# Kernel tuning notes

Measured on AMD Instinct MI355X. Metric: run time of the kernel, lower is better.

The kernel has to match this reference:

```python
import jax, jax.numpy as jnp
import numpy as np

DIM = 1024
N_HEADS = 16
HEAD_DIM = DIM // N_HEADS
MAX_SEQ = 2048
B, S = 4, 2048


def _rope_tables(seq_len):
    inv_freq = 1.0 / (10000.0 ** (jnp.arange(0, HEAD_DIM, 2, dtype=jnp.float32) / HEAD_DIM))
    t = jnp.arange(seq_len, dtype=jnp.float32)
    freqs = jnp.outer(t, inv_freq)            # [S, HEAD_DIM/2]
    emb = jnp.concatenate([freqs, freqs], -1)  # [S, HEAD_DIM]
    return jnp.cos(emb), jnp.sin(emb)


def _apply_rope(x, cos, sin):
    # x: [B, S, H, Dh]; cos/sin: [S, Dh]
    c = cos[None, :, None, :]
    s = sin[None, :, None, :]
    x1, x2 = jnp.split(x, 2, axis=-1)
    x_rot = jnp.concatenate([-x2, x1], -1)
    return x * c + x_rot * s


def setup_inputs() -> dict:
    key = jax.random.key(0)
    kx, kq, kk, kv, ko = jax.random.split(key, 5)
    std = DIM ** -0.5
    x = jax.random.normal(kx, (B, S, DIM), jnp.float32)
    Wq = jax.random.normal(kq, (DIM, DIM), jnp.float32) * std
    Wk = jax.random.normal(kk, (DIM, DIM), jnp.float32) * std
    Wv = jax.random.normal(kv, (DIM, DIM), jnp.float32) * std
    Wo = jax.random.normal(ko, (DIM, DIM), jnp.float32) * std
    # causal mask: 1 where attending is allowed, 0 where masked (mask==0 -> -inf)
    mask = jnp.tril(jnp.ones((S, S), jnp.int32))[None, None]  # [1,1,S,S]
    return {"x": x, "Wq": Wq, "Wk": Wk, "Wv": Wv, "Wo": Wo, "mask": mask}


def reference(x, Wq, Wk, Wv, Wo, mask) -> jnp.ndarray:
    b, s, _ = x.shape
    scale = HEAD_DIM ** -0.5
    # torch Linear: y = x @ W.T, W is [out, in]
    q = (x @ Wq.T).reshape(b, s, N_HEADS, HEAD_DIM)
    k = (x @ Wk.T).reshape(b, s, N_HEADS, HEAD_DIM)
    v = (x @ Wv.T).reshape(b, s, N_HEADS, HEAD_DIM)
    cos, sin = _rope_tables(s)
    q = _apply_rope(q, cos, sin)
    k = _apply_rope(k, cos, sin)
    # [B, H, S, S]
    attn = jnp.einsum('bqhd,bkhd->bhqk', q, k) * scale
    attn = jnp.where(mask == 0, -jnp.inf, attn)
    attn = jax.nn.softmax(attn, axis=-1)
    out = jnp.einsum('bhqk,bkhd->bqhd', attn, v).reshape(b, s, DIM)
    return out @ Wo.T
```

## Files before the change

### kernel.cpp

```cpp
#include <hip/hip_runtime.h>
#include <hip/hip_bf16.h>
#include <math.h>

using bf16 = __hip_bfloat16;
typedef __attribute__((ext_vector_type(8))) short short8;
typedef __attribute__((ext_vector_type(4))) float float4v;

#define DIM 1024
#define NH 16
#define HD 64
#define BB 4
#define SS 2048
#define MTOT (BB * SS)

#define ROPE_LOG2 0.41524101186092034f
#define PC1 0.18033688f
#define PC0 -23.08312066f

__device__ inline short bf16bits(float x) {
  return __builtin_bit_cast(short, __float2bfloat16(x));
}
__device__ inline float bits2f(unsigned short b) {
  return __builtin_bit_cast(float, (unsigned)b << 16);
}
__device__ inline unsigned pack2(float a, float b) {
  return (unsigned)(unsigned short)bf16bits(a) |
         ((unsigned)(unsigned short)bf16bits(b) << 16);
}

__device__ inline void async16(const void* g, void* l) {
  __builtin_amdgcn_global_load_lds(
      (const __attribute__((address_space(1))) void*)g,
      (__attribute__((address_space(3))) void*)l, 16, 0, 0);
}

__device__ inline void cvt8(const float* __restrict__ in, bf16* __restrict__ out,
                            size_t i) {
  const float4v* p = (const float4v*)in + i * 2;
  float4v a = p[0], b = p[1];
  short8 r;
  r[0] = bf16bits(a[0]); r[1] = bf16bits(a[1]);
  r[2] = bf16bits(a[2]); r[3] = bf16bits(a[3]);
  r[4] = bf16bits(b[0]); r[5] = bf16bits(b[1]);
  r[6] = bf16bits(b[2]); r[7] = bf16bits(b[3]);
  ((short8*)out)[i] = r;
}

__global__ __launch_bounds__(256) void prep(
    const float* __restrict__ x, const float* __restrict__ w0,
    const float* __restrict__ w1, const float* __restrict__ w2,
    const float* __restrict__ w3, bf16* __restrict__ xb, bf16* __restrict__ o0,
    bf16* __restrict__ o1, bf16* __restrict__ o2, bf16* __restrict__ o3,
    unsigned* __restrict__ tab) {
  const int bid = blockIdx.x;
  const int tid = threadIdx.x;
  if (bid < 4096) {
    cvt8(x, xb, (size_t)bid * 256 + tid);
  } else if (bid < 6144) {
    int wsel = (bid - 4096) >> 9;
    const float* in = wsel == 0 ? w0 : wsel == 1 ? w1 : wsel == 2 ? w2 : w3;
    bf16* out = wsel == 0 ? o0 : wsel == 1 ? o1 : wsel == 2 ? o2 : o3;
    cvt8(in, out, (size_t)((bid - 4096) & 511) * 256 + tid);
  } else {
    int i = (bid - 6144) * 256 + tid;
    int s = i >> 5, d = i & 31;
    float inv = exp2f(-(float)d * ROPE_LOG2);
    float sn, cs;
    sincosf((float)s * inv, &sn, &cs);
    tab[i] = pack2(cs, sn);
  }
}

__global__ __launch_bounds__(256, 3) void gemm_qkv(
    const bf16* __restrict__ A, const bf16* __restrict__ W,
    bf16* __restrict__ Cbase, const unsigned* __restrict__ rt) {
  __shared__ __align__(16) short sPool[4][4096];
  short* sT = &sPool[0][0];

  const int tid = threadIdx.x;
  const int wave = tid >> 6;
  const int lane = tid & 63;
  const int l15 = lane & 15;
  const int quad = lane >> 4;
  const int m0 = blockIdx.x * 128;
  const int n0 = blockIdx.y * 128;
  const int wm = (wave >> 1) * 64;
  const int wn = (wave & 1) * 64;
  const int K = DIM;

  float4v acc[4][4];
#pragma unroll
  for (int i = 0; i < 4; i++)
#pragma unroll
    for (int j = 0; j < 4; j++)
#pragma unroll
      for (int r = 0; r < 4; r++) acc[i][j][r] = 0.0f;

  auto stage = [&](int buf, int k0) {
    short* dA = &sPool[buf * 2][0];
    short* dB = &sPool[buf * 2 + 1][0];
#pragma unroll
    for (int i = 0; i < 2; i++) {
      int c0 = i * 256 + wave * 64;
      int c = c0 + lane;
      int row = c >> 2, cb = c & 3;
      async16(A + (size_t)(m0 + row) * K + k0 + cb * 8, dA + c0 * 8);
      async16(W + (size_t)(n0 + row) * K + k0 + cb * 8, dB + c0 * 8);
    }
  };

  stage(0, 0);
  __syncthreads();

  int cur = 0;
  for (int k0 = 0; k0 < K; k0 += 32, cur ^= 1) {
    if (k0 + 32 < K) stage(cur ^ 1, k0 + 32);

    const short* sA = &sPool[cur * 2][0];
    const short* sB = &sPool[cur * 2 + 1][0];
    short8 af[4], bfr[4];
#pragma unroll
    for (int mi = 0; mi < 4; mi++)
      af[mi] = *(const short8*)(sA + (wm + mi * 16 + l15) * 32 + quad * 8);
#pragma unroll
    for (int ni = 0; ni < 4; ni++)
      bfr[ni] = *(const short8*)(sB + (wn + ni * 16 + l15) * 32 + quad * 8);
#pragma unroll
    for (int mi = 0; mi < 4; mi++)
#pragma unroll
      for (int ni = 0; ni < 4; ni++)
        acc[mi][ni] = __builtin_amdgcn_mfma_f32_16x16x32_bf16(
            af[mi], bfr[ni], acc[mi][ni], 0, 0, 0);

    __syncthreads();
  }

  const int third = n0 >> 10;
  const int nloc = n0 & 1023;
  bf16* C = Cbase + (size_t)third * MTOT * DIM;

  if (third == 2) {
    const int bb_ = m0 >> 11;
    const int s0 = m0 & (SS - 1);
    const int h0 = nloc >> 6;
#pragma unroll
    for (int half = 0; half < 2; half++) {
      if (half) __syncthreads();
      if ((wave & 1) == half) {
#pragma unroll
        for (int mi = 0; mi < 4; mi++)
#pragma unroll
          for (int ni = 0; ni < 4; ni++)
#pragma unroll
            for (int r = 0; r < 4; r++)
              sT[(ni * 16 + l15) * 130 + wm + mi * 16 + quad * 4 + r] =
                  bf16bits(acc[mi][ni][r]);
      }
      __syncthreads();
      int row = tid >> 2, cb = tid & 3;
      size_t base =
          ((size_t)(bb_ * NH + h0 + half) * HD + row) * SS + s0 + cb * 32;
#pragma unroll
      for (int c = 0; c < 4; c++) {
        short8 vv = *(const short8*)(sT + row * 130 + cb * 32 + c * 8);
        *(short8*)((short*)C + base + c * 8) = vv;
      }
    }
    return;
  }

#pragma unroll
  for (int mi = 0; mi < 4; mi++) {
#pragma unroll
    for (int r = 0; r < 4; r++) {
      int m = m0 + wm + mi * 16 + quad * 4 + r;
      int b = m >> 11;
      int s = m & (SS - 1);
      int h = (nloc + wn) >> 6;
      bf16* outp = C + ((size_t)(b * NH + h) * SS + s) * HD;
#pragma unroll
      for (int ni = 0; ni < 2; ni++) {
        int d = ni * 16 + l15;
        unsigned cspack = rt[s * 32 + d];
        float cs = bits2f((unsigned short)(cspack & 0xffff));
        float sn = bits2f((unsigned short)(cspack >> 16));
        float lo = acc[mi][ni][r];
        float hi = acc[mi][ni + 2][r];
        outp[d] = __float2bfloat16(lo * cs - hi * sn);
        outp[d + 32] = __float2bfloat16(hi * cs + lo * sn);
      }
    }
  }
}

__global__ __launch_bounds__(256, 3) void gemm_out(const bf16* __restrict__ A,
                                                   const bf16* __restrict__ W,
                                                   float* __restrict__ C) {
  __shared__ __align__(16) short sPool[4][4096];

  const int tid = threadIdx.x;
  const int wave = tid >> 6;
  const int lane = tid & 63;
  const int l15 = lane & 15;
  const int quad = lane >> 4;
  const int m0 = blockIdx.x * 128;
  const int n0 = blockIdx.y * 128;
  const int wm = (wave >> 1) * 64;
  const int wn = (wave & 1) * 64;
  const int K = DIM, N = DIM;

  float4v acc[4][4];
#pragma unroll
  for (int i = 0; i < 4; i++)
#pragma unroll
    for (int j = 0; j < 4; j++)
#pragma unroll
      for (int r = 0; r < 4; r++) acc[i][j][r] = 0.0f;

  auto stage = [&](int buf, int k0) {
    short* dA = &sPool[buf * 2][0];
    short* dB = &sPool[buf * 2 + 1][0];
#pragma unroll
    for (int i = 0; i < 2; i++) {
      int c0 = i * 256 + wave * 64;
      int c = c0 + lane;
      int row = c >> 2, cb = c & 3;
      async16(A + (size_t)(m0 + row) * K + k0 + cb * 8, dA + c0 * 8);
      async16(W + (size_t)(n0 + row) * K + k0 + cb * 8, dB + c0 * 8);
    }
  };

  stage(0, 0);
  __syncthreads();

  int cur = 0;
  for (int k0 = 0; k0 < K; k0 += 32, cur ^= 1) {
    if (k0 + 32 < K) stage(cur ^ 1, k0 + 32);

    const short* sA = &sPool[cur * 2][0];
    const short* sB = &sPool[cur * 2 + 1][0];
    short8 af[4], bfr[4];
#pragma unroll
    for (int mi = 0; mi < 4; mi++)
      af[mi] = *(const short8*)(sA + (wm + mi * 16 + l15) * 32 + quad * 8);
#pragma unroll
    for (int ni = 0; ni < 4; ni++)
      bfr[ni] = *(const short8*)(sB + (wn + ni * 16 + l15) * 32 + quad * 8);
#pragma unroll
    for (int mi = 0; mi < 4; mi++)
#pragma unroll
      for (int ni = 0; ni < 4; ni++)
        acc[mi][ni] = __builtin_amdgcn_mfma_f32_16x16x32_bf16(
            af[mi], bfr[ni], acc[mi][ni], 0, 0, 0);

    __syncthreads();
  }

#pragma unroll
  for (int mi = 0; mi < 4; mi++) {
#pragma unroll
    for (int r = 0; r < 4; r++) {
      int m = m0 + wm + mi * 16 + quad * 4 + r;
#pragma unroll
      for (int ni = 0; ni < 4; ni++) {
        int n = n0 + wn + ni * 16 + l15;
        C[(size_t)m * N + n] = acc[mi][ni][r];
      }
    }
  }
}

#define SKV 64
#define SP 64

__global__ __launch_bounds__(512, 2) void attn_fwd(const bf16* __restrict__ q,
                                                   const bf16* __restrict__ k,
                                                   const bf16* __restrict__ vt,
                                                   bf16* __restrict__ o) {
  __shared__ __align__(16) short sK[2][64 * SKV];
  __shared__ __align__(16) short sV[2][64 * SKV];
  __shared__ __align__(16) short sP[8][16 * SP];

  const int tid = threadIdx.x;
  const int wave = tid >> 6;
  const int g = wave >> 2;
  const int wv = wave & 3;
  const int lane = tid & 63;
  const int l15 = lane & 15;
  const int quad = lane >> 4;
  const int bh = blockIdx.x;
  const int p = blockIdx.y;
  const int qt[4] = {g == 0 ? p : 7 - p, g == 0 ? 15 - p : 8 + p,
                     g == 0 ? 16 + p : 23 - p, g == 0 ? 31 - p : 24 + p};
  const int maxkt = 31 - p;
  const size_t hb = (size_t)bh * SS * HD;
  const size_t vtb = (size_t)bh * HD * SS;

  short8 aQ[4][2];
#pragma unroll
  for (int ti = 0; ti < 4; ti++) {
    const bf16* qp =
        q + hb + (size_t)(qt[ti] * 64 + wv * 16 + l15) * HD + quad * 8;
    aQ[ti][0] = *(const short8*)qp;
    aQ[ti][1] = *(const short8*)(qp + 32);
  }

  float l_part[4] = {0.0f, 0.0f, 0.0f, 0.0f};
  float4v acc_o[4][4];
#pragma unroll
  for (int ti = 0; ti < 4; ti++)
#pragma unroll
    for (int di = 0; di < 4; di++)
#pragma unroll
      for (int r = 0; r < 4; r++) acc_o[ti][di][r] = 0.0f;

  int4 kr, vr;
  auto load_kv = [&](int kt_) {
    int k0n = kt_ * 64;
    int c = tid;
    kr = *(const int4*)(k + hb + (size_t)(k0n + (c >> 3)) * HD + (c & 7) * 8);
    vr = *(const int4*)(vt + vtb + (size_t)(c >> 3) * SS + k0n + (c & 7) * 8);
  };
  auto stage_write = [&](int buf) {
    int c = tid;
    int row = c >> 3;
    int sl = (c & 7) ^ (row & 7);
    *(int4*)(&sK[buf][row * SKV + sl * 8]) = kr;
    *(int4*)(&sV[buf][row * SKV + sl * 8]) = vr;
  };

  load_kv(0);
  stage_write(0);
  __syncthreads();

  for (int kt = 0; kt <= maxkt; kt++) {
    const int cur = kt & 1;
    if (kt < maxkt) load_kv(kt + 1);

    short8 kf[8], vf[8];
#pragma unroll
    for (int t = 0; t < 2; t++)
#pragma unroll
      for (int i = 0; i < 4; i++) {
        int row = i * 16 + l15;
        int sl = (t * 4 + quad) ^ (l15 & 7);
        kf[t * 4 + i] = *(const short8*)(&sK[cur][row * SKV + sl * 8]);
        vf[t * 4 + i] = *(const short8*)(&sV[cur][row * SKV + sl * 8]);
      }

    const int k0 = kt * 64;
    short* pw = &sP[wave][0];
#pragma unroll
    for (int ti = 0; ti < 4; ti++) {
      if (kt <= qt[ti]) {
        float4v s[4];
#pragma unroll
        for (int ni = 0; ni < 4; ni++)
#pragma unroll
          for (int r = 0; r < 4; r++) s[ni][r] = 0.0f;
        __builtin_amdgcn_s_setprio(1);
#pragma unroll
        for (int t = 0; t < 2; t++)
#pragma unroll
          for (int ni = 0; ni < 4; ni++)
            s[ni] = __builtin_amdgcn_mfma_f32_16x16x32_bf16(
                kf[t * 4 + ni], aQ[ti][t], s[ni], 0, 0, 0);
        __builtin_amdgcn_s_setprio(0);

        const bool diag = (kt == qt[ti]);
        const int qglob = qt[ti] * 64 + wv * 16 + l15;
#pragma unroll
        for (int ni = 0; ni < 4; ni++) {
          float pe[4];
#pragma unroll
          for (int r = 0; r < 4; r++) {
            float x = exp2f(fmaf(s[ni][r], PC1, PC0));
            if (diag && (k0 + ni * 16 + quad * 4 + r > qglob)) x = 0.0f;
            l_part[ti] += x;
            pe[r] = x;
          }
          int2 w2;
          w2.x = (int)pack2(pe[0], pe[1]);
          w2.y = (int)pack2(pe[2], pe[3]);
          int slw = (2 * ni + (quad >> 1)) ^ (l15 & 7);
          *(int2*)(pw + l15 * SP + slw * 8 + (quad & 1) * 4) = w2;
        }
        asm volatile("s_waitcnt lgkmcnt(0)" ::: "memory");

        __builtin_amdgcn_s_setprio(1);
#pragma unroll
        for (int t = 0; t < 2; t++) {
          int slr = (t * 4 + quad) ^ (l15 & 7);
          short8 aP = *(const short8*)(pw + l15 * SP + slr * 8);
#pragma unroll
          for (int di = 0; di < 4; di++)
            acc_o[ti][di] = __builtin_amdgcn_mfma_f32_16x16x32_bf16(
                aP, vf[t * 4 + di], acc_o[ti][di], 0, 0, 0);
        }
        __builtin_amdgcn_s_setprio(0);
      }
    }

    if (kt < maxkt) stage_write(cur ^ 1);
    __syncthreads();
  }

  const int b = bh >> 4, h = bh & 15;
#pragma unroll
  for (int ti = 0; ti < 4; ti++) {
    float lr = l_part[ti];
    lr += __shfl_xor(lr, 16, 64);
    lr += __shfl_xor(lr, 32, 64);
#pragma unroll
    for (int r = 0; r < 4; r++) {
      float invl = 1.0f / __shfl(lr, quad * 4 + r, 64);
      bf16* op =
          o + (size_t)(b * SS + qt[ti] * 64 + wv * 16 + quad * 4 + r) * DIM +
          h * HD;
#pragma unroll
      for (int di = 0; di < 4; di++)
        op[di * 16 + l15] = __float2bfloat16(acc_o[ti][di][r] * invl);
    }
  }
}

extern "C" void kernel_launch(void* const* d_in, const int* in_sizes, int n_in,
                              void* d_out, int out_size, void* d_ws,
                              size_t ws_size, hipStream_t stream) {
  const float* x = (const float*)d_in[0];
  const float* Wq = (const float*)d_in[1];
  const float* Wk = (const float*)d_in[2];
  const float* Wv = (const float*)d_in[3];
  const float* Wo = (const float*)d_in[4];
  float* out = (float*)d_out;

  char* ws = (char*)d_ws;
  const size_t xsz = (size_t)MTOT * DIM * sizeof(bf16);
  bf16* xb = (bf16*)ws;
  bf16* qb_ = (bf16*)(ws + xsz);
  bf16* kb = (bf16*)(ws + 2 * xsz);
  bf16* vtb = (bf16*)(ws + 3 * xsz);
  bf16* wqb = (bf16*)(ws + 4 * xsz);
  bf16* wkb = wqb + (size_t)DIM * DIM;
  bf16* wvb = wkb + (size_t)DIM * DIM;
  bf16* wob = wvb + (size_t)DIM * DIM;
  unsigned* rt = (unsigned*)(wob + (size_t)DIM * DIM);
  bf16* ob = xb;

  dim3 bb(256);
  prep<<<dim3(6400), bb, 0, stream>>>(x, Wq, Wk, Wv, Wo, xb, wqb, wkb, wvb,
                                      wob, rt);
  gemm_qkv<<<dim3(MTOT / 128, 3 * DIM / 128), bb, 0, stream>>>(xb, wqb, qb_,
                                                               rt);
  attn_fwd<<<dim3(BB * NH, 4), dim3(512), 0, stream>>>(qb_, kb, vtb, ob);
  gemm_out<<<dim3(MTOT / 128, DIM / 128), bb, 0, stream>>>(ob, wob, out);
}
```

Before: 269.4 us.

## Enlarge QKV GEMM tiles to 256x256 with swizzled LDS and split-phase pipelining

```diff
diff --git a/kernel.cpp b/kernel.cpp
--- a/kernel.cpp
+++ b/kernel.cpp
@@ -71,68 +71,91 @@
   }
 }
 
-__global__ __launch_bounds__(256, 3) void gemm_qkv(
+__global__ __launch_bounds__(512, 2) void gemm_qkv(
     const bf16* __restrict__ A, const bf16* __restrict__ W,
     bf16* __restrict__ Cbase, const unsigned* __restrict__ rt) {
-  __shared__ __align__(16) short sPool[4][4096];
-  short* sT = &sPool[0][0];
+  __shared__ __align__(16) short sPool[32768];
 
   const int tid = threadIdx.x;
   const int wave = tid >> 6;
+  const int wm2 = wave >> 2;
+  const int wn4 = wave & 3;
   const int lane = tid & 63;
   const int l15 = lane & 15;
   const int quad = lane >> 4;
-  const int m0 = blockIdx.x * 128;
-  const int n0 = blockIdx.y * 128;
-  const int wm = (wave >> 1) * 64;
-  const int wn = (wave & 1) * 64;
-  const int K = DIM;
-
-  float4v acc[4][4];
-#pragma unroll
-  for (int i = 0; i < 4; i++)
+  const int sw2 = (l15 >> 1) & 3;
+  const int NKT = DIM / 32;
+
+  const int bid = blockIdx.x;
+  const int swz = (bid & 7) * 48 + (bid >> 3);
+  const int m0 = (swz / 12) * 256;
+  const int n0 = (swz % 12) * 256;
+
+  float4v acc[8][4];
+#pragma unroll
+  for (int i = 0; i < 8; i++)
 #pragma unroll
     for (int j = 0; j < 4; j++)
 #pragma unroll
       for (int r = 0; r < 4; r++) acc[i][j][r] = 0.0f;
 
-  auto stage = [&](int buf, int k0) {
-    short* dA = &sPool[buf * 2][0];
-    short* dB = &sPool[buf * 2 + 1][0];
-#pragma unroll
-    for (int i = 0; i < 2; i++) {
-      int c0 = i * 256 + wave * 64;
-      int c = c0 + lane;
-      int row = c >> 2, cb = c & 3;
-      async16(A + (size_t)(m0 + row) * K + k0 + cb * 8, dA + c0 * 8);
-      async16(W + (size_t)(n0 + row) * K + k0 + cb * 8, dB + c0 * 8);
-    }
+  auto stageu = [&](int kt_, int h) {
+    int c = tid;
+    int rl = c >> 2;
+    int sl = (c & 3) ^ ((c >> 3) & 3);
+    int row = ((h & 1) << 7) + rl;
+    const bf16* src = (h < 2)
+        ? A + (size_t)(m0 + row) * DIM + kt_ * 32 + sl * 8
+        : W + (size_t)(n0 + row) * DIM + kt_ * 32 + sl * 8;
+    async16(src, sPool + (kt_ & 1) * 16384 + h * 4096 + wave * 512);
   };
 
-  stage(0, 0);
-  __syncthreads();
-
-  int cur = 0;
-  for (int k0 = 0; k0 < K; k0 += 32, cur ^= 1) {
-    if (k0 + 32 < K) stage(cur ^ 1, k0 + 32);
-
-    const short* sA = &sPool[cur * 2][0];
-    const short* sB = &sPool[cur * 2 + 1][0];
-    short8 af[4], bfr[4];
-#pragma unroll
-    for (int mi = 0; mi < 4; mi++)
-      af[mi] = *(const short8*)(sA + (wm + mi * 16 + l15) * 32 + quad * 8);
-#pragma unroll
-    for (int ni = 0; ni < 4; ni++)
-      bfr[ni] = *(const short8*)(sB + (wn + ni * 16 + l15) * 32 + quad * 8);
+  stageu(0, 0); stageu(0, 1); stageu(0, 2); stageu(0, 3);
+  stageu(1, 0); stageu(1, 1); stageu(1, 2);
+  asm volatile("s_waitcnt vmcnt(3)" ::: "memory");
+  __builtin_amdgcn_s_barrier();
+
+  for (int kt = 0; kt < NKT; kt++) {
+    const short* bufp = sPool + (kt & 1) * 16384;
+    short8 af[8], bfr[4];
+#pragma unroll
+    for (int mi = 0; mi < 8; mi++) {
+      int row = wm2 * 128 + mi * 16 + l15;
+      af[mi] = *(const short8*)(bufp + row * 32 + (quad ^ sw2) * 8);
+    }
+#pragma unroll
+    for (int ni = 0; ni < 4; ni++) {
+      int row = wn4 * 64 + ni * 16 + l15;
+      bfr[ni] = *(const short8*)(bufp + 8192 + row * 32 + (quad ^ sw2) * 8);
+    }
+    if (kt + 1 < NKT) stageu(kt + 1, 3);
+    __builtin_amdgcn_s_setprio(1);
 #pragma unroll
     for (int mi = 0; mi < 4; mi++)
 #pragma unroll
       for (int ni = 0; ni < 4; ni++)
         acc[mi][ni] = __builtin_amdgcn_mfma_f32_16x16x32_bf16(
             af[mi], bfr[ni], acc[mi][ni], 0, 0, 0);
-
-    __syncthreads();
+    __builtin_amdgcn_s_setprio(0);
+    asm volatile("s_waitcnt lgkmcnt(0)" ::: "memory");
+    __builtin_amdgcn_s_barrier();
+
+    if (kt + 2 < NKT) { stageu(kt + 2, 0); stageu(kt + 2, 1); stageu(kt + 2, 2); }
+    __builtin_amdgcn_s_setprio(1);
+#pragma unroll
+    for (int mi = 4; mi < 8; mi++)
+#pragma unroll
+      for (int ni = 0; ni < 4; ni++)
+        acc[mi][ni] = __builtin_amdgcn_mfma_f32_16x16x32_bf16(
+            af[mi], bfr[ni], acc[mi][ni], 0, 0, 0);
+    __builtin_amdgcn_s_setprio(0);
+    if (kt < NKT - 1) {
+      if (kt + 2 < NKT)
+        asm volatile("s_waitcnt vmcnt(3)" ::: "memory");
+      else
+        asm volatile("s_waitcnt vmcnt(0)" ::: "memory");
+      __builtin_amdgcn_s_barrier();
+    }
   }
 
   const int third = n0 >> 10;
@@ -140,43 +163,42 @@
   bf16* C = Cbase + (size_t)third * MTOT * DIM;
 
   if (third == 2) {
-    const int bb_ = m0 >> 11;
+    const int b_ = m0 >> 11;
     const int s0 = m0 & (SS - 1);
-    const int h0 = nloc >> 6;
-#pragma unroll
-    for (int half = 0; half < 2; half++) {
-      if (half) __syncthreads();
-      if ((wave & 1) == half) {
-#pragma unroll
-        for (int mi = 0; mi < 4; mi++)
+    short* sT = sPool;
+#pragma unroll 1
+    for (int hp = 0; hp < 4; hp++) {
+      __syncthreads();
+      if (wn4 == hp) {
+#pragma unroll
+        for (int mi = 0; mi < 8; mi++)
 #pragma unroll
           for (int ni = 0; ni < 4; ni++)
 #pragma unroll
             for (int r = 0; r < 4; r++)
-              sT[(ni * 16 + l15) * 130 + wm + mi * 16 + quad * 4 + r] =
+              sT[(ni * 16 + l15) * 264 + wm2 * 128 + mi * 16 + quad * 4 + r] =
                   bf16bits(acc[mi][ni][r]);
       }
       __syncthreads();
-      int row = tid >> 2, cb = tid & 3;
-      size_t base =
-          ((size_t)(bb_ * NH + h0 + half) * HD + row) * SS + s0 + cb * 32;
-#pragma unroll
-      for (int c = 0; c < 4; c++) {
-        short8 vv = *(const short8*)(sT + row * 130 + cb * 32 + c * 8);
-        *(short8*)((short*)C + base + c * 8) = vv;
-      }
+      int hglob = (nloc >> 6) + hp;
+      int d = tid >> 3, ch = tid & 7;
+      size_t base = ((size_t)(b_ * NH + hglob) * HD + d) * SS + s0 + ch * 32;
+      const short* srow = sT + d * 264 + ch * 32;
+#pragma unroll
+      for (int j = 0; j < 4; j++)
+        *(short8*)((short*)C + base + j * 8) = *(const short8*)(srow + j * 8);
     }
     return;
   }
 
-#pragma unroll
-  for (int mi = 0; mi < 4; mi++) {
+  const int h = (nloc >> 6) + wn4;
+#pragma unroll
+  for (int mi = 0; mi < 8; mi++) {
 #pragma unroll
     for (int r = 0; r < 4; r++) {
-      int m = m0 + wm + mi * 16 + quad * 4 + r;
+      int m = m0 + wm2 * 128 + mi * 16 + quad * 4 + r;
       int b = m >> 11;
       int s = m & (SS - 1);
-      int h = (nloc + wn) >> 6;
       bf16* outp = C + ((size_t)(b * NH + h) * SS + s) * HD;
 #pragma unroll
       for (int ni = 0; ni < 2; ni++) {
@@ -450,8 +472,7 @@
   dim3 bb(256);
   prep<<<dim3(6400), bb, 0, stream>>>(x, Wq, Wk, Wv, Wo, xb, wqb, wkb, wvb,
                                       wob, rt);
-  gemm_qkv<<<dim3(MTOT / 128, 3 * DIM / 128), bb, 0, stream>>>(xb, wqb, qb_,
-                                                               rt);
+  gemm_qkv<<<dim3(384), dim3(512), 0, stream>>>(xb, wqb, qb_, rt);
   attn_fwd<<<dim3(BB * NH, 4), dim3(512), 0, stream>>>(qb_, kb, vtb, ob);
   gemm_out<<<dim3(MTOT / 128, DIM / 128), bb, 0, stream>>>(ob, wob, out);
 }
```

After: 277.5 us. 3.0% more time.
